# Performance work log

Measured on AMD Instinct MI355X. Metric: run time of the kernel, lower is better.

## Reference

```python
import jax, jax.numpy as jnp
import numpy as np

RATIO = 4


def setup_inputs() -> dict:
    key = jax.random.key(0)
    ks = jax.random.split(key, 6)
    b, c, hw = 8, 64, 256
    n = (hw // RATIO) ** 2  # 4096
    return {
        "x": jax.random.normal(ks[0], (b, c, hw, hw), dtype=jnp.float32),
        "weight": jax.random.normal(ks[1], (n, n), dtype=jnp.float32) * 0.01,
        "pih_w": jax.random.normal(ks[2], (c, c, 3, 3), dtype=jnp.float32) * 0.05,
        "pih_b": jax.random.normal(ks[3], (c,), dtype=jnp.float32) * 0.05,
        "up_w": jax.random.normal(ks[4], (c, c, 4, 4), dtype=jnp.float32) * 0.05,
        "up_b": jax.random.normal(ks[5], (c,), dtype=jnp.float32) * 0.05,
    }


def reference(x, weight, pih_w, pih_b, up_w, up_b):
    b, c, h, w = x.shape
    identity = x
    # MaxPool2d(ratio)
    xp = jax.lax.reduce_window(x, -jnp.inf, jax.lax.max,
                               (1, 1, RATIO, RATIO), (1, 1, RATIO, RATIO), 'VALID')
    # 3x3 conv, pad 1
    x_pih = jax.lax.conv_general_dilated(
        xp, pih_w, window_strides=(1, 1), padding='SAME',
        dimension_numbers=('NCHW', 'OIHW', 'NCHW')) + pih_b[None, :, None, None]
    x_pih = jax.nn.relu(x_pih).reshape(b, c, -1)  # [b, c, N]
    # F.normalize(p=2, dim=2)
    nrm = jnp.sqrt(jnp.sum(x_pih * x_pih, axis=2, keepdims=True))
    nx = x_pih / jnp.maximum(nrm, 1e-12)
    # channel-channel affinity [b, c, c]
    A = jnp.einsum('bcn,bdn->bcd', nx, nx)
    # vectorized D^{-1/2}, replacing per-batch torch.diag loop
    d = 1.0 / jnp.sqrt(jnp.sum(A, axis=2) + 1e-8)  # [b, c]
    d = jnp.where(jnp.isfinite(d), d, 0.0)
    L = jnp.eye(c, dtype=x.dtype)[None] - d[:, :, None] * A * d[:, None, :]
    # diffusion: L @ x_flat @ W
    xf = xp.reshape(b, c, -1)  # [b, c, N]
    out = jnp.einsum('bcd,bdn->bcn', L, xf)
    out = jnp.einsum('bcn,nm->bcm', out, weight)
    hp, wp = h // RATIO, w // RATIO
    out = out.reshape(b, c, hp, wp)
    # ConvTranspose2d(k=4, s=4): each pixel expands to a 4x4 block
    up = jnp.einsum('bchw,coij->bohiwj', out, up_w).reshape(b, c, h, w)
    up = up + up_b[None, :, None, None]
    return jax.nn.relu(up + identity)
```

## Files before the change

### kernel.cpp

```cpp
#include <hip/hip_runtime.h>

#define NB 8
#define NC 64
#define HW 256
#define HP 64
#define NN 4096

typedef unsigned short u16;
typedef unsigned int u32;
typedef __attribute__((ext_vector_type(8))) short s16x8;
typedef __attribute__((ext_vector_type(8))) unsigned short u16x8;
typedef __attribute__((ext_vector_type(4))) float f32x4;

__device__ __forceinline__ u16 f2bf(float f) {
    unsigned u = __float_as_uint(f);
    return (u16)((u + 0x7fffu + ((u >> 16) & 1u)) >> 16);
}
__device__ __forceinline__ float bf2f(u16 v) {
    return __uint_as_float(((unsigned)v) << 16);
}

#define GLOAD16(gsrc, ldst) \
    __builtin_amdgcn_global_load_lds((const __attribute__((address_space(1))) unsigned int*)(gsrc), \
                                     (__attribute__((address_space(3))) unsigned int*)(ldst), 16, 0, 0)

__global__ __launch_bounds__(256) void maxpool_nhwc_k(const float* __restrict__ x,
                                                      u16* __restrict__ xpc) {
    __shared__ u16 tile[64 * 66];
    int bid = blockIdx.x;
    int b = bid >> 6, y = bid & 63;
    int t = threadIdx.x;
    int cl  = t >> 3;
    int seg = t & 7;
#pragma unroll
    for (int pass = 0; pass < 2; ++pass) {
        int c = pass * 32 + cl;
        const float* p = x + ((long)(b * 64 + c) * 256 + y * 4) * 256 + seg * 32;
        float m[8];
#pragma unroll
        for (int i = 0; i < 8; ++i) m[i] = -3.4e38f;
#pragma unroll
        for (int r = 0; r < 4; ++r)
#pragma unroll
            for (int i = 0; i < 8; ++i) {
                float4 v = *(const float4*)(p + r * 256 + i * 4);
                m[i] = fmaxf(m[i], fmaxf(fmaxf(v.x, v.y), fmaxf(v.z, v.w)));
            }
#pragma unroll
        for (int i = 0; i < 8; ++i) tile[c * 66 + seg * 8 + i] = f2bf(m[i]);
    }
    __syncthreads();
    int xo = t >> 2, cp = t & 3;
    u16x8 o0, o1;
#pragma unroll
    for (int e = 0; e < 8; ++e) o0[e] = tile[(cp * 16 + e) * 66 + xo];
#pragma unroll
    for (int e = 0; e < 8; ++e) o1[e] = tile[(cp * 16 + 8 + e) * 66 + xo];
    u16* dst = xpc + ((long)(b * 4096 + y * 64 + xo)) * 64 + cp * 16;
    *(u16x8*)dst = o0;
    *(u16x8*)(dst + 8) = o1;
}

__global__ __launch_bounds__(256) void transWb_k(const float* __restrict__ W,
                                                 u16* __restrict__ WTb) {
    __shared__ float tile[64 * 65];
    int k0 = blockIdx.x * 64;
    int n0 = blockIdx.y * 64;
    int t = threadIdx.x;
#pragma unroll
    for (int i = 0; i < 4; ++i) {
        int idx = t + i * 256;
        int r  = idx >> 4;
        int c4 = (idx & 15) * 4;
        float4 v = *(const float4*)&W[(long)(k0 + r) * 4096 + n0 + c4];
        tile[(c4 + 0) * 65 + r] = v.x;
        tile[(c4 + 1) * 65 + r] = v.y;
        tile[(c4 + 2) * 65 + r] = v.z;
        tile[(c4 + 3) * 65 + r] = v.w;
    }
    __syncthreads();
#pragma unroll
    for (int i = 0; i < 2; ++i) {
        int chunk = t + i * 256;
        int nr = chunk >> 3;
        int kc = (chunk & 7) * 8;
        u16x8 o;
#pragma unroll
        for (int j = 0; j < 8; ++j) o[j] = f2bf(tile[nr * 65 + kc + j]);
        *(u16x8*)&WTb[(long)(n0 + nr) * 4096 + k0 + kc] = o;
    }
}

__global__ __launch_bounds__(256) void prep_k(const float* __restrict__ uw,
                                              const float* __restrict__ pw,
                                              u16* __restrict__ Wb,
                                              u16* __restrict__ Bpack) {
    int bid = blockIdx.x;
    int t = threadIdx.x;
    if (bid < 256) {
        int idx = bid * 256 + t;
        int c = idx & 63;
        int n = idx >> 6;
        int o = n >> 4, i = (n >> 2) & 3, j = n & 3;
        Wb[idx] = f2bf(uw[((c * 64 + o) * 4 + i) * 4 + j]);
    } else {
        int idx = (bid - 256) * 256 + t;
        if (idx >= 36864) return;
        int e = idx & 7, l = (idx >> 3) & 63, nf = (idx >> 9) & 3, s = idx >> 11;
        int ch = s & 1, kd = s >> 1;
        int dy = kd / 3, dx = kd % 3;
        int o  = nf * 16 + (l & 15);
        int ci = ch * 32 + (l >> 4) * 8 + e;
        Bpack[idx] = f2bf(pw[((o * 64 + ci) * 3 + dy) * 3 + dx]);
    }
}

__global__ __launch_bounds__(256) void convgram_k(const u16* __restrict__ xpc,
                                                  const u16* __restrict__ Bpack,
                                                  const float* __restrict__ pb,
                                                  float* __restrict__ G) {
    __shared__ alignas(16) u16 ldsIn[3 * 66 * 64];
    __shared__ alignas(16) u16 ldsX[64 * 64];
    int bid = blockIdx.x;
    int b = bid >> 6, y = bid & 63;
    int t = threadIdx.x;
    int w = t >> 6, l = t & 63;
    int lr = l & 15, ksub = l >> 4;

    if (t < 48) {
        int r = t >> 4, q = t & 15;
        int off = r * 8448 + (q < 8 ? q * 16 : 8320 + (q - 8) * 16);
        *(u16x8*)((char*)ldsIn + off) = (u16x8){0, 0, 0, 0, 0, 0, 0, 0};
    }
#pragma unroll
    for (int i = 0; i < 6; ++i) {
        int r  = i >> 1;
        int ya = y - 1 + r;
        int wro = (i & 1) * 4096 + t * 16;
        int dst = r * 8448 + 128 + wro;
        if (ya >= 0 && ya < 64) {
            int xsl = 1 + (wro >> 7);
            int srcoff = (wro & ~127) | ((wro & 127) ^ ((xsl & 7) << 4));
            GLOAD16((const char*)xpc + (long)(b * 64 + ya) * 8192 + srcoff,
                    (char*)ldsIn + dst);
        } else {
            *(u16x8*)((char*)ldsIn + dst) = (u16x8){0, 0, 0, 0, 0, 0, 0, 0};
        }
    }
    __syncthreads();

    f32x4 acc[4];
#pragma unroll
    for (int mf = 0; mf < 4; ++mf) acc[mf] = (f32x4){0.f, 0.f, 0.f, 0.f};

#pragma unroll
    for (int kd = 0; kd < 9; ++kd) {
        int dy = kd / 3, dx = kd % 3;
#pragma unroll
        for (int ch = 0; ch < 2; ++ch) {
            int s = kd * 2 + ch;
            s16x8 bfrag = *(const s16x8*)(Bpack + ((s * 4 + w) * 64 + l) * 8);
#pragma unroll
            for (int mf = 0; mf < 4; ++mf) {
                int xsl  = mf * 16 + lr + dx;
                int coff = (ch * 64 + ksub * 16) ^ ((xsl & 7) << 4);
                s16x8 af = *(const s16x8*)((const char*)ldsIn +
                                           dy * 8448 + xsl * 128 + coff);
                acc[mf] = __builtin_amdgcn_mfma_f32_16x16x32_bf16(
                    af, bfrag, acc[mf], 0, 0, 0);
            }
        }
    }
    int o = w * 16 + lr;
    float bias = pb[o];
#pragma unroll
    for (int mf = 0; mf < 4; ++mf)
#pragma unroll
        for (int rp = 0; rp < 2; ++rp) {
            u16 lo = f2bf(fmaxf(acc[mf][rp * 2]     + bias, 0.f));
            u16 hi = f2bf(fmaxf(acc[mf][rp * 2 + 1] + bias, 0.f));
            int nb   = (mf * 16 + ksub * 4 + rp * 2) * 2;
            int boff = nb ^ ((o & 7) << 4);
            *(u32*)((char*)ldsX + o * 128 + boff) = (u32)lo | ((u32)hi << 16);
        }
    __syncthreads();

    f32x4 g[4];
#pragma unroll
    for (int nf = 0; nf < 4; ++nf) g[nf] = (f32x4){0.f, 0.f, 0.f, 0.f};
#pragma unroll
    for (int kk = 0; kk < 2; ++kk) {
        int kb = kk * 64 + ksub * 16;
        int arow = w * 16 + lr;
        s16x8 af = *(const s16x8*)((const char*)ldsX + arow * 128 +
                                   (kb ^ ((arow & 7) << 4)));
#pragma unroll
        for (int nf = 0; nf < 4; ++nf) {
            int brow = nf * 16 + lr;
            s16x8 bf = *(const s16x8*)((const char*)ldsX + brow * 128 +
                                       (kb ^ ((brow & 7) << 4)));
            g[nf] = __builtin_amdgcn_mfma_f32_16x16x32_bf16(af, bf, g[nf], 0, 0, 0);
        }
    }
    float* Gb = G + b * 4096;
#pragma unroll
    for (int nf = 0; nf < 4; ++nf)
#pragma unroll
        for (int r = 0; r < 4; ++r)
            atomicAdd(&Gb[(w * 16 + ksub * 4 + r) * 64 + nf * 16 + lr], g[nf][r]);
}

__global__ __launch_bounds__(256) void diffuse_mfma_k(const float* __restrict__ G,
                                                      const u16* __restrict__ xpc,
                                                      u16* __restrict__ Ab16) {
    __shared__ alignas(16) u16 lds[128 * 64];
    __shared__ alignas(16) u16 ldsL[64 * 64];
    __shared__ float nrm[64], dvv[64];
    int n0 = blockIdx.x * 128;
    int b  = blockIdx.y;
    int t = threadIdx.x;
    int w = t >> 6, l = t & 63;
    int lr = l & 15, ksub = l >> 4;

#pragma unroll
    for (int i = 0; i < 4; ++i) {
        int d = i * 4096 + t * 16;
        int row = d >> 7, off = d & 127;
        GLOAD16((const char*)xpc + ((long)(b * 4096 + n0 + row)) * 128 +
                (off ^ ((row & 7) << 4)),
                (char*)lds + d);
    }

    const float* Gb = G + b * 4096;
    if (t < 64) nrm[t] = fmaxf(sqrtf(Gb[t * 64 + t]), 1e-12f);
    __syncthreads();
    if (t < 64) {
        float nc = nrm[t];
        float rs = 0.f;
        for (int d = 0; d < 64; ++d) rs += Gb[t * 64 + d] / (nc * nrm[d]);
        float dd = 1.0f / sqrtf(rs + 1e-8f);
        if (!(dd <= 3.0e38f)) dd = 0.0f;
        dvv[t] = dd;
    }
    __syncthreads();
    {
        int c = t >> 2;
        int dbase = (t & 3) * 16;
        float nc = nrm[c], dc = dvv[c];
#pragma unroll
        for (int dp2 = 0; dp2 < 8; ++dp2) {
            int d0 = dbase + dp2 * 2;
            float A0 = Gb[c * 64 + d0]     / (nc * nrm[d0]);
            float A1 = Gb[c * 64 + d0 + 1] / (nc * nrm[d0 + 1]);
            float v0 = ((c == d0)     ? 1.f : 0.f) - dc * A0 * dvv[d0];
            float v1 = ((c == d0 + 1) ? 1.f : 0.f) - dc * A1 * dvv[d0 + 1];
            int o = c * 64 + (d0 ^ ((c & 7) << 3));
            *(u32*)&ldsL[o] = (u32)f2bf(v0) | ((u32)f2bf(v1) << 16);
        }
    }
    __syncthreads();

    f32x4 acc[4][2];
#pragma unroll
    for (int mf = 0; mf < 4; ++mf)
#pragma unroll
        for (int nq = 0; nq < 2; ++nq) acc[mf][nq] = (f32x4){0.f, 0.f, 0.f, 0.f};

#pragma unroll
    for (int kk = 0; kk < 2; ++kk) {
        s16x8 bfr[2];
#pragma unroll
        for (int nq = 0; nq < 2; ++nq) {
            int brow = w * 32 + nq * 16 + lr;
            bfr[nq] = *(const s16x8*)((const char*)lds + brow * 128 +
                                      ((kk * 64 + ksub * 16) ^ ((brow & 7) << 4)));
        }
#pragma unroll
        for (int mf = 0; mf < 4; ++mf) {
            int arow = mf * 16 + lr;
            s16x8 af = *(const s16x8*)((const char*)ldsL + arow * 128 +
                                       ((kk * 64 + ksub * 16) ^ ((arow & 7) << 4)));
#pragma unroll
            for (int nq = 0; nq < 2; ++nq)
                acc[mf][nq] = __builtin_amdgcn_mfma_f32_16x16x32_bf16(
                    af, bfr[nq], acc[mf][nq], 0, 0, 0);
        }
    }
#pragma unroll
    for (int mf = 0; mf < 4; ++mf)
#pragma unroll
        for (int nq = 0; nq < 2; ++nq)
#pragma unroll
            for (int r = 0; r < 4; ++r)
                Ab16[((long)(b * 64 + mf * 16 + (l >> 4) * 4 + r)) * 4096 +
                     n0 + w * 32 + nq * 16 + lr] = f2bf(acc[mf][nq][r]);
}

#define KSPLIT 4
#define KSLICE 1024
__global__ __launch_bounds__(256) void gemm_mfma_k(const u16* __restrict__ A,
                                                   const u16* __restrict__ WT,
                                                   u16* __restrict__ Cp) {
    __shared__ alignas(16) u16 ldsA[8192];
    __shared__ alignas(16) u16 ldsB[8192];
    int bid = blockIdx.x;
    int swz = (bid & 7) * 64 + (bid >> 3);
    int m0 = (swz & 3) * 128;
    int n0 = ((swz >> 2) & 31) * 128;
    int z  = swz >> 7;
    int t = threadIdx.x;
    int w = t >> 6, l = t & 63;
    int wr = w >> 1, wc = w & 1;
    int lr = l & 15;
    int lk = (l >> 4) << 4;

    f32x4 acc[4][4];
#pragma unroll
    for (int mf = 0; mf < 4; ++mf)
#pragma unroll
        for (int nf = 0; nf < 4; ++nf) acc[mf][nf] = (f32x4){0.f, 0.f, 0.f, 0.f};

    const char* Ab = (const char*)(A  + (long)m0 * 4096 + z * KSLICE);
    const char* Bb = (const char*)(WT + (long)n0 * 4096 + z * KSLICE);

    for (int k0 = 0; k0 < KSLICE; k0 += 64) {
        __syncthreads();
#pragma unroll
        for (int i = 0; i < 4; ++i) {
            int d   = i * 4096 + t * 16;
            int row = d >> 7;
            int off = d & 127;
            int sk  = off ^ ((row & 7) << 4);
            GLOAD16(Ab + (long)row * 8192 + k0 * 2 + sk, (char*)ldsA + d);
            GLOAD16(Bb + (long)row * 8192 + k0 * 2 + sk, (char*)ldsB + d);
        }
        __syncthreads();
#pragma unroll
        for (int kk = 0; kk < 2; ++kk) {
            s16x8 af[4], bf[4];
#pragma unroll
            for (int f = 0; f < 4; ++f) {
                int ar = wr * 64 + f * 16 + lr;
                af[f] = *(const s16x8*)((const char*)ldsA + ar * 128 +
                                        ((kk * 64 + lk) ^ ((ar & 7) << 4)));
                int br = wc * 64 + f * 16 + lr;
                bf[f] = *(const s16x8*)((const char*)ldsB + br * 128 +
                                        ((kk * 64 + lk) ^ ((br & 7) << 4)));
            }
#pragma unroll
            for (int mf = 0; mf < 4; ++mf)
#pragma unroll
                for (int nf = 0; nf < 4; ++nf)
                    acc[mf][nf] = __builtin_amdgcn_mfma_f32_16x16x32_bf16(
                        af[mf], bf[nf], acc[mf][nf], 0, 0, 0);
        }
    }
    int tile = (swz & 3) * 32 + ((swz >> 2) & 31);
    u16 carr[64];
#pragma unroll
    for (int mf = 0; mf < 4; ++mf)
#pragma unroll
        for (int nf = 0; nf < 4; ++nf)
#pragma unroll
            for (int r = 0; r < 4; ++r)
                carr[mf * 16 + nf * 4 + r] = f2bf(acc[mf][nf][r]);
    u16* dp = Cp + ((long)(z * 128 + tile) * 256 + t) * 64;
#pragma unroll
    for (int v8 = 0; v8 < 8; ++v8)
        *(u16x8*)&dp[v8 * 8] = *(const u16x8*)&carr[v8 * 8];
}

__global__ __launch_bounds__(256) void reduce4T_k(const u16* __restrict__ Cp,
                                                  u16* __restrict__ A2) {
    __shared__ u16 ldsT[128 * 128];
    int tile = blockIdx.x;
    int tm = tile >> 5, tn = tile & 31;
    int n0 = tn * 128;
    int t = threadIdx.x;
    int w = t >> 6, l = t & 63;
    int wr = w >> 1, wc = w & 1, lr = l & 15;

    float s[64];
#pragma unroll
    for (int k = 0; k < 64; ++k) s[k] = 0.f;

    const u16* dp = Cp + ((long)tile * 256 + t) * 64;
#pragma unroll
    for (int z = 0; z < KSPLIT; ++z) {
        const u16* pz = dp + (long)z * 128 * 256 * 64;
#pragma unroll
        for (int v8 = 0; v8 < 8; ++v8) {
            u16x8 vv = *(const u16x8*)&pz[v8 * 8];
#pragma unroll
            for (int e = 0; e < 8; ++e) s[v8 * 8 + e] += bf2f(vv[e]);
        }
    }
#pragma unroll
    for (int mf = 0; mf < 4; ++mf)
#pragma unroll
        for (int nf = 0; nf < 4; ++nf) {
            int mbase = wr * 64 + mf * 16 + (l >> 4) * 4;
            int pix   = wc * 64 + nf * 16 + lr;
            int g = (mbase >> 3) ^ (pix & 7);
            int o = pix * 128 + g * 8 + (mbase & 7);
            u32 w0 = (u32)f2bf(s[mf * 16 + nf * 4 + 0]) |
                     ((u32)f2bf(s[mf * 16 + nf * 4 + 1]) << 16);
            u32 w1 = (u32)f2bf(s[mf * 16 + nf * 4 + 2]) |
                     ((u32)f2bf(s[mf * 16 + nf * 4 + 3]) << 16);
            *(u32*)&ldsT[o]     = w0;
            *(u32*)&ldsT[o + 2] = w1;
        }
    __syncthreads();
    int pix_l = t >> 1, bh = t & 1;
    u16* dst = A2 + ((long)((2 * tm + bh) * 4096 + n0 + pix_l)) * 64;
#pragma unroll
    for (int gg = 0; gg < 8; ++gg) {
        int q = bh * 8 + gg;
        u16x8 vv = *(const u16x8*)&ldsT[pix_l * 128 + (q ^ (pix_l & 7)) * 8];
        *(u16x8*)&dst[gg * 8] = vv;
    }
}

__global__ __launch_bounds__(256) void convT_mfma_k(const u16* __restrict__ A2,
                                                    const u16* __restrict__ Wb,
                                                    const float* __restrict__ ub,
                                                    const float* __restrict__ x,
                                                    float* __restrict__ out) {
    __shared__ alignas(16) char smem[34816];
    u16*   ldsA = (u16*)smem;
    u16*   ldsB = (u16*)(smem + 16384);
    float* ldsC = (float*)smem;
    int mt = blockIdx.x;
    int nt = blockIdx.y;
    int m0 = mt * 128;
    int n0 = nt * 128;
    int t = threadIdx.x;
    int w = t >> 6, l = t & 63;
    int wr = w >> 1, wc = w & 1;
    int lr = l & 15;
    int lkb = (l >> 4) << 4;

    const char* Ab = (const char*)(A2 + (long)m0 * 64);
    const char* Bb = (const char*)(Wb + (long)n0 * 64);
#pragma unroll
    for (int i = 0; i < 4; ++i) {
        int d = i * 4096 + t * 16;
        int srcoff = (d & ~127) | ((d & 127) ^ (((d >> 7) & 7) << 4));
        GLOAD16(Ab + srcoff, (char*)ldsA + d);
        GLOAD16(Bb + srcoff, (char*)ldsB + d);
    }
    __syncthreads();

    f32x4 acc[4][4];
#pragma unroll
    for (int mf = 0; mf < 4; ++mf)
#pragma unroll
        for (int nf = 0; nf < 4; ++nf) acc[mf][nf] = (f32x4){0.f, 0.f, 0.f, 0.f};

#pragma unroll
    for (int kk = 0; kk < 2; ++kk) {
        s16x8 af[4], bfg[4];
#pragma unroll
        for (int f = 0; f < 4; ++f) {
            int ar = wr * 64 + f * 16 + lr;
            af[f] = *(const s16x8*)((const char*)ldsA + ar * 128 +
                                    ((kk * 64 + lkb) ^ ((ar & 7) << 4)));
            int br = wc * 64 + f * 16 + lr;
            bfg[f] = *(const s16x8*)((const char*)ldsB + br * 128 +
                                     ((kk * 64 + lkb) ^ ((br & 7) << 4)));
        }
#pragma unroll
        for (int mf = 0; mf < 4; ++mf)
#pragma unroll
            for (int nf = 0; nf < 4; ++nf)
                acc[mf][nf] = __builtin_amdgcn_mfma_f32_16x16x32_bf16(
                    af[mf], bfg[nf], acc[mf][nf], 0, 0, 0);
    }
    __syncthreads();

#pragma unroll
    for (int nh = 0; nh < 2; ++nh) {
        if (nh) __syncthreads();
        if (wc == nh) {
#pragma unroll
            for (int mf = 0; mf < 4; ++mf)
#pragma unroll
                for (int nf = 0; nf < 4; ++nf)
#pragma unroll
                    for (int r = 0; r < 4; ++r) {
                        int row = wr * 64 + mf * 16 + (l >> 4) * 4 + r;
                        int col = nf * 16 + lr;
                        ldsC[row * 68 + (col ^ (((row >> 3) & 7) << 2))] =
                            acc[mf][nf][r];
                    }
        }
        __syncthreads();
#pragma unroll
        for (int q = 0; q < 2; ++q) {
            int idx = q * 256 + t;
            int ml = idx & 127;
            int oo = idx >> 7;
            int o  = nt * 8 + nh * 4 + oo;
            float bias = ub[o];
            int mg = m0 + ml;
            int b = mg >> 12, pix = mg & 4095;
            int h = pix >> 6, ww = pix & 63;
            long base = ((long)(b * 64 + o) * 256 + h * 4) * 256 + ww * 4;
#pragma unroll
            for (int i = 0; i < 4; ++i) {
                f32x4 cv = *(const f32x4*)&ldsC[ml * 68 +
                            ((oo * 16 + i * 4) ^ (((ml >> 3) & 7) << 2))];
                float4 xi = *(const float4*)&x[base + i * 256];
                float4 rr;
                rr.x = fmaxf(cv[0] + bias + xi.x, 0.f);
                rr.y = fmaxf(cv[1] + bias + xi.y, 0.f);
                rr.z = fmaxf(cv[2] + bias + xi.z, 0.f);
                rr.w = fmaxf(cv[3] + bias + xi.w, 0.f);
                *(float4*)&out[base + i * 256] = rr;
            }
        }
    }
}

extern "C" void kernel_launch(void* const* d_in, const int* in_sizes, int n_in,
                              void* d_out, int out_size, void* d_ws, size_t ws_size,
                              hipStream_t stream) {
    const float* x      = (const float*)d_in[0];
    const float* weight = (const float*)d_in[1];
    const float* pih_w  = (const float*)d_in[2];
    const float* pih_b  = (const float*)d_in[3];
    const float* up_w   = (const float*)d_in[4];
    const float* up_b   = (const float*)d_in[5];
    float* out = (float*)d_out;
    float* ws  = (float*)d_ws;

    u16*   xpc   = (u16*)ws;
    u16*   Ab16  = (u16*)(ws + 3145728);
    float* G     = ws + 4194304;
    u16*   Wb    = (u16*)(ws + 4259840);
    u16*   WTb   = (u16*)(ws + 4325376);
    u16*   Cp    = (u16*)(ws + 12713984);
    u16*   Bpack = Cp + 2097152;
    u16*   A2    = (u16*)ws;

    hipMemsetAsync(G, 0, 32768 * sizeof(float), stream);
    maxpool_nhwc_k<<<512, 256, 0, stream>>>(x, xpc);
    transWb_k     <<<dim3(64, 64), 256, 0, stream>>>(weight, WTb);
    prep_k        <<<400, 256, 0, stream>>>(up_w, pih_w, Wb, Bpack);
    convgram_k    <<<512, 256, 0, stream>>>(xpc, Bpack, pih_b, G);
    diffuse_mfma_k<<<dim3(32, 8), 256, 0, stream>>>(G, xpc, Ab16);
    gemm_mfma_k   <<<512, 256, 0, stream>>>(Ab16, WTb, Cp);
    reduce4T_k    <<<128, 256, 0, stream>>>(Cp, A2);
    convT_mfma_k  <<<dim3(256, 8), 256, 0, stream>>>(A2, Wb, up_b, x, out);
}
```

Before: 168.0 us.

## Merge prep kernels into one launch and fold split-K reduction into convT

Merges the maxpool, weight transpose and parameter-packing kernels into a single launch that picks its role from the block index. Removes the separate split-K reduce/transpose kernel: each convT block now sums the bf16 partial products straight from the Cp buffer and writes the swizzled A tile into LDS, so the A2 intermediate is no longer written and read back. Adds a block-index swizzle to the convT grid, which would otherwise read each Cp tile repeatedly across the 8 n-tiles; the swizzle is meant to keep those re-reads close together in time so they hit cache. The trade-off is that the split-K partials are now re-read by every n-tile block instead of once.

```diff
diff --git a/kernel.cpp b/kernel.cpp
--- a/kernel.cpp
+++ b/kernel.cpp
@@ -24,94 +24,94 @@
     __builtin_amdgcn_global_load_lds((const __attribute__((address_space(1))) unsigned int*)(gsrc), \
                                      (__attribute__((address_space(3))) unsigned int*)(ldst), 16, 0, 0)
 
-__global__ __launch_bounds__(256) void maxpool_nhwc_k(const float* __restrict__ x,
-                                                      u16* __restrict__ xpc) {
-    __shared__ u16 tile[64 * 66];
-    int bid = blockIdx.x;
-    int b = bid >> 6, y = bid & 63;
-    int t = threadIdx.x;
-    int cl  = t >> 3;
-    int seg = t & 7;
-#pragma unroll
-    for (int pass = 0; pass < 2; ++pass) {
-        int c = pass * 32 + cl;
-        const float* p = x + ((long)(b * 64 + c) * 256 + y * 4) * 256 + seg * 32;
-        float m[8];
-#pragma unroll
-        for (int i = 0; i < 8; ++i) m[i] = -3.4e38f;
-#pragma unroll
-        for (int r = 0; r < 4; ++r)
-#pragma unroll
-            for (int i = 0; i < 8; ++i) {
-                float4 v = *(const float4*)(p + r * 256 + i * 4);
-                m[i] = fmaxf(m[i], fmaxf(fmaxf(v.x, v.y), fmaxf(v.z, v.w)));
-            }
-#pragma unroll
-        for (int i = 0; i < 8; ++i) tile[c * 66 + seg * 8 + i] = f2bf(m[i]);
-    }
-    __syncthreads();
-    int xo = t >> 2, cp = t & 3;
-    u16x8 o0, o1;
-#pragma unroll
-    for (int e = 0; e < 8; ++e) o0[e] = tile[(cp * 16 + e) * 66 + xo];
-#pragma unroll
-    for (int e = 0; e < 8; ++e) o1[e] = tile[(cp * 16 + 8 + e) * 66 + xo];
-    u16* dst = xpc + ((long)(b * 4096 + y * 64 + xo)) * 64 + cp * 16;
-    *(u16x8*)dst = o0;
-    *(u16x8*)(dst + 8) = o1;
-}
-
-__global__ __launch_bounds__(256) void transWb_k(const float* __restrict__ W,
-                                                 u16* __restrict__ WTb) {
-    __shared__ float tile[64 * 65];
-    int k0 = blockIdx.x * 64;
-    int n0 = blockIdx.y * 64;
-    int t = threadIdx.x;
-#pragma unroll
-    for (int i = 0; i < 4; ++i) {
-        int idx = t + i * 256;
-        int r  = idx >> 4;
-        int c4 = (idx & 15) * 4;
-        float4 v = *(const float4*)&W[(long)(k0 + r) * 4096 + n0 + c4];
-        tile[(c4 + 0) * 65 + r] = v.x;
-        tile[(c4 + 1) * 65 + r] = v.y;
-        tile[(c4 + 2) * 65 + r] = v.z;
-        tile[(c4 + 3) * 65 + r] = v.w;
-    }
-    __syncthreads();
-#pragma unroll
-    for (int i = 0; i < 2; ++i) {
-        int chunk = t + i * 256;
-        int nr = chunk >> 3;
-        int kc = (chunk & 7) * 8;
-        u16x8 o;
-#pragma unroll
-        for (int j = 0; j < 8; ++j) o[j] = f2bf(tile[nr * 65 + kc + j]);
-        *(u16x8*)&WTb[(long)(n0 + nr) * 4096 + k0 + kc] = o;
-    }
-}
-
-__global__ __launch_bounds__(256) void prep_k(const float* __restrict__ uw,
-                                              const float* __restrict__ pw,
-                                              u16* __restrict__ Wb,
-                                              u16* __restrict__ Bpack) {
+__global__ __launch_bounds__(256) void front_k(const float* __restrict__ x,
+                                               const float* __restrict__ W,
+                                               const float* __restrict__ uw,
+                                               const float* __restrict__ pw,
+                                               u16* __restrict__ xpc,
+                                               u16* __restrict__ WTb,
+                                               u16* __restrict__ Wb,
+                                               u16* __restrict__ Bpack) {
+    __shared__ alignas(16) char sm[16640];
     int bid = blockIdx.x;
     int t = threadIdx.x;
-    if (bid < 256) {
-        int idx = bid * 256 + t;
-        int c = idx & 63;
-        int n = idx >> 6;
-        int o = n >> 4, i = (n >> 2) & 3, j = n & 3;
-        Wb[idx] = f2bf(uw[((c * 64 + o) * 4 + i) * 4 + j]);
+    if (bid < 512) {
+        u16* tile = (u16*)sm;
+        int b = bid >> 6, y = bid & 63;
+        int cl  = t >> 3;
+        int seg = t & 7;
+#pragma unroll
+        for (int pass = 0; pass < 2; ++pass) {
+            int c = pass * 32 + cl;
+            const float* p = x + ((long)(b * 64 + c) * 256 + y * 4) * 256 + seg * 32;
+            float m[8];
+#pragma unroll
+            for (int i = 0; i < 8; ++i) m[i] = -3.4e38f;
+#pragma unroll
+            for (int r = 0; r < 4; ++r)
+#pragma unroll
+                for (int i = 0; i < 8; ++i) {
+                    float4 v = *(const float4*)(p + r * 256 + i * 4);
+                    m[i] = fmaxf(m[i], fmaxf(fmaxf(v.x, v.y), fmaxf(v.z, v.w)));
+                }
+#pragma unroll
+            for (int i = 0; i < 8; ++i) tile[c * 66 + seg * 8 + i] = f2bf(m[i]);
+        }
+        __syncthreads();
+        int xo = t >> 2, cp = t & 3;
+        u16x8 o0, o1;
+#pragma unroll
+        for (int e = 0; e < 8; ++e) o0[e] = tile[(cp * 16 + e) * 66 + xo];
+#pragma unroll
+        for (int e = 0; e < 8; ++e) o1[e] = tile[(cp * 16 + 8 + e) * 66 + xo];
+        u16* dst = xpc + ((long)(b * 4096 + y * 64 + xo)) * 64 + cp * 16;
+        *(u16x8*)dst = o0;
+        *(u16x8*)(dst + 8) = o1;
+    } else if (bid < 4608) {
+        float* tile = (float*)sm;
+        int tb = bid - 512;
+        int k0 = (tb & 63) * 64;
+        int n0 = (tb >> 6) * 64;
+#pragma unroll
+        for (int i = 0; i < 4; ++i) {
+            int idx = t + i * 256;
+            int r  = idx >> 4;
+            int c4 = (idx & 15) * 4;
+            float4 v = *(const float4*)&W[(long)(k0 + r) * 4096 + n0 + c4];
+            tile[(c4 + 0) * 65 + r] = v.x;
+            tile[(c4 + 1) * 65 + r] = v.y;
+            tile[(c4 + 2) * 65 + r] = v.z;
+            tile[(c4 + 3) * 65 + r] = v.w;
+        }
+        __syncthreads();
+#pragma unroll
+        for (int i = 0; i < 2; ++i) {
+            int chunk = t + i * 256;
+            int nr = chunk >> 3;
+            int kc = (chunk & 7) * 8;
+            u16x8 o;
+#pragma unroll
+            for (int j = 0; j < 8; ++j) o[j] = f2bf(tile[nr * 65 + kc + j]);
+            *(u16x8*)&WTb[(long)(n0 + nr) * 4096 + k0 + kc] = o;
+        }
     } else {
-        int idx = (bid - 256) * 256 + t;
-        if (idx >= 36864) return;
-        int e = idx & 7, l = (idx >> 3) & 63, nf = (idx >> 9) & 3, s = idx >> 11;
-        int ch = s & 1, kd = s >> 1;
-        int dy = kd / 3, dx = kd % 3;
-        int o  = nf * 16 + (l & 15);
-        int ci = ch * 32 + (l >> 4) * 8 + e;
-        Bpack[idx] = f2bf(pw[((o * 64 + ci) * 3 + dy) * 3 + dx]);
+        int pbid = bid - 4608;
+        if (pbid < 256) {
+            int idx = pbid * 256 + t;
+            int c = idx & 63;
+            int n = idx >> 6;
+            int o = n >> 4, i = (n >> 2) & 3, j = n & 3;
+            Wb[idx] = f2bf(uw[((c * 64 + o) * 4 + i) * 4 + j]);
+        } else {
+            int idx = (pbid - 256) * 256 + t;
+            if (idx >= 36864) return;
+            int e = idx & 7, l = (idx >> 3) & 63, nf = (idx >> 9) & 3, s = idx >> 11;
+            int ch = s & 1, kd = s >> 1;
+            int dy = kd / 3, dx = kd % 3;
+            int o  = nf * 16 + (l & 15);
+            int ci = ch * 32 + (l >> 4) * 8 + e;
+            Bpack[idx] = f2bf(pw[((o * 64 + ci) * 3 + dy) * 3 + dx]);
+        }
     }
 }
 
@@ -370,58 +370,7 @@
         *(u16x8*)&dp[v8 * 8] = *(const u16x8*)&carr[v8 * 8];
 }
 
-__global__ __launch_bounds__(256) void reduce4T_k(const u16* __restrict__ Cp,
-                                                  u16* __restrict__ A2) {
-    __shared__ u16 ldsT[128 * 128];
-    int tile = blockIdx.x;
-    int tm = tile >> 5, tn = tile & 31;
-    int n0 = tn * 128;
-    int t = threadIdx.x;
-    int w = t >> 6, l = t & 63;
-    int wr = w >> 1, wc = w & 1, lr = l & 15;
-
-    float s[64];
-#pragma unroll
-    for (int k = 0; k < 64; ++k) s[k] = 0.f;
-
-    const u16* dp = Cp + ((long)tile * 256 + t) * 64;
-#pragma unroll
-    for (int z = 0; z < KSPLIT; ++z) {
-        const u16* pz = dp + (long)z * 128 * 256 * 64;
-#pragma unroll
-        for (int v8 = 0; v8 < 8; ++v8) {
-            u16x8 vv = *(const u16x8*)&pz[v8 * 8];
-#pragma unroll
-            for (int e = 0; e < 8; ++e) s[v8 * 8 + e] += bf2f(vv[e]);
-        }
-    }
-#pragma unroll
-    for (int mf = 0; mf < 4; ++mf)
-#pragma unroll
-        for (int nf = 0; nf < 4; ++nf) {
-            int mbase = wr * 64 + mf * 16 + (l >> 4) * 4;
-            int pix   = wc * 64 + nf * 16 + lr;
-            int g = (mbase >> 3) ^ (pix & 7);
-            int o = pix * 128 + g * 8 + (mbase & 7);
-            u32 w0 = (u32)f2bf(s[mf * 16 + nf * 4 + 0]) |
-                     ((u32)f2bf(s[mf * 16 + nf * 4 + 1]) << 16);
-            u32 w1 = (u32)f2bf(s[mf * 16 + nf * 4 + 2]) |
-                     ((u32)f2bf(s[mf * 16 + nf * 4 + 3]) << 16);
-            *(u32*)&ldsT[o]     = w0;
-            *(u32*)&ldsT[o + 2] = w1;
-        }
-    __syncthreads();
-    int pix_l = t >> 1, bh = t & 1;
-    u16* dst = A2 + ((long)((2 * tm + bh) * 4096 + n0 + pix_l)) * 64;
-#pragma unroll
-    for (int gg = 0; gg < 8; ++gg) {
-        int q = bh * 8 + gg;
-        u16x8 vv = *(const u16x8*)&ldsT[pix_l * 128 + (q ^ (pix_l & 7)) * 8];
-        *(u16x8*)&dst[gg * 8] = vv;
-    }
-}
-
-__global__ __launch_bounds__(256) void convT_mfma_k(const u16* __restrict__ A2,
+__global__ __launch_bounds__(256) void convT_mfma_k(const u16* __restrict__ Cp,
                                                     const u16* __restrict__ Wb,
                                                     const float* __restrict__ ub,
                                                     const float* __restrict__ x,
@@ -430,8 +379,10 @@
     u16*   ldsA = (u16*)smem;
     u16*   ldsB = (u16*)(smem + 16384);
     float* ldsC = (float*)smem;
-    int mt = blockIdx.x;
-    int nt = blockIdx.y;
+    int bid = blockIdx.x;
+    int swzb = (bid & 7) * 256 + (bid >> 3);
+    int mt = swzb >> 3;
+    int nt = swzb & 7;
     int m0 = mt * 128;
     int n0 = nt * 128;
     int t = threadIdx.x;
@@ -440,14 +391,53 @@
     int lr = l & 15;
     int lkb = (l >> 4) << 4;
 
-    const char* Ab = (const char*)(A2 + (long)m0 * 64);
     const char* Bb = (const char*)(Wb + (long)n0 * 64);
 #pragma unroll
     for (int i = 0; i < 4; ++i) {
         int d = i * 4096 + t * 16;
         int srcoff = (d & ~127) | ((d & 127) ^ (((d >> 7) & 7) << 4));
-        GLOAD16(Ab + srcoff, (char*)ldsA + d);
         GLOAD16(Bb + srcoff, (char*)ldsB + d);
+    }
+
+    {
+        int b_   = mt >> 5;
+        int wr_g = b_ & 1;
+        int tile_g = (b_ >> 1) * 32 + (mt & 31);
+        int tg = wr_g * 128 + (t & 127);
+        int h  = t >> 7;
+        int l_g = tg & 63, wc_g = (tg >> 6) & 1;
+        int k4 = l_g >> 4, lr_g = l_g & 15;
+        float s[32];
+#pragma unroll
+        for (int k = 0; k < 32; ++k) s[k] = 0.f;
+        const u16* dpb = Cp + ((long)tile_g * 256 + tg) * 64 + h * 32;
+#pragma unroll
+        for (int z = 0; z < KSPLIT; ++z) {
+            const u16* pz = dpb + (long)z * 2097152;
+#pragma unroll
+            for (int j = 0; j < 4; ++j) {
+                u16x8 vv = *(const u16x8*)&pz[j * 8];
+#pragma unroll
+                for (int e = 0; e < 8; ++e) s[j * 8 + e] += bf2f(vv[e]);
+            }
+        }
+#pragma unroll
+        for (int j = 0; j < 4; ++j) {
+            int v8 = h * 4 + j;
+            int mf = v8 >> 1;
+            int c0 = mf * 16 + k4 * 4;
+#pragma unroll
+            for (int q = 0; q < 2; ++q) {
+                int nf  = (v8 & 1) * 2 + q;
+                int pix = wc_g * 64 + nf * 16 + lr_g;
+                int sw  = (pix & 7) << 4;
+                int f   = j * 8 + q * 4;
+                u32 w0 = (u32)f2bf(s[f + 0]) | ((u32)f2bf(s[f + 1]) << 16);
+                u32 w1 = (u32)f2bf(s[f + 2]) | ((u32)f2bf(s[f + 3]) << 16);
+                *(u32*)((char*)ldsA + pix * 128 + ((c0 * 2) ^ sw))     = w0;
+                *(u32*)((char*)ldsA + pix * 128 + ((c0 * 2 + 4) ^ sw)) = w1;
+            }
+        }
     }
     __syncthreads();
 
@@ -504,8 +494,8 @@
             float bias = ub[o];
             int mg = m0 + ml;
             int b = mg >> 12, pix = mg & 4095;
-            int h = pix >> 6, ww = pix & 63;
-            long base = ((long)(b * 64 + o) * 256 + h * 4) * 256 + ww * 4;
+            int h2 = pix >> 6, ww = pix & 63;
+            long base = ((long)(b * 64 + o) * 256 + h2 * 4) * 256 + ww * 4;
 #pragma unroll
             for (int i = 0; i < 4; ++i) {
                 f32x4 cv = *(const f32x4*)&ldsC[ml * 68 +
@@ -541,15 +531,12 @@
     u16*   WTb   = (u16*)(ws + 4325376);
     u16*   Cp    = (u16*)(ws + 12713984);
     u16*   Bpack = Cp + 2097152;
-    u16*   A2    = (u16*)ws;
 
     hipMemsetAsync(G, 0, 32768 * sizeof(float), stream);
-    maxpool_nhwc_k<<<512, 256, 0, stream>>>(x, xpc);
-    transWb_k     <<<dim3(64, 64), 256, 0, stream>>>(weight, WTb);
-    prep_k        <<<400, 256, 0, stream>>>(up_w, pih_w, Wb, Bpack);
+    front_k       <<<5008, 256, 0, stream>>>(x, weight, up_w, pih_w,
+                                             xpc, WTb, Wb, Bpack);
     convgram_k    <<<512, 256, 0, stream>>>(xpc, Bpack, pih_b, G);
     diffuse_mfma_k<<<dim3(32, 8), 256, 0, stream>>>(G, xpc, Ab16);
     gemm_mfma_k   <<<512, 256, 0, stream>>>(Ab16, WTb, Cp);
-    reduce4T_k    <<<128, 256, 0, stream>>>(Cp, A2);
-    convT_mfma_k  <<<dim3(256, 8), 256, 0, stream>>>(A2, Wb, up_b, x, out);
-}
+    convT_mfma_k  <<<2048, 256, 0, stream>>>(Cp, Wb, up_b, x, out);
+}
```

New measurement: 160.7 us. 1.05x faster.

## Merge maxpool, weight transpose and prep into one front kernel; swizzle convT grid

Applied to the files above, without the earlier changes.

Folds the three independent preprocessing kernels (maxpool to NHWC bf16, weight transpose to bf16, and conv/convT weight packing) into one launch that dispatches by block index range. The weight transpose now uses 128x128 tiles with an XOR-swizzled bf16 LDS tile, packing to bf16 before staging, in place of the fp32 padded tile. The convT kernel moves to a 1D grid whose block-to-tile mapping is remapped so that blocks running at the same time spread over more M tiles. The aim is to cut launch gaps and the transpose's LDS traffic, at the cost of a heterogeneous kernel whose shared-memory footprint is sized for its largest branch.

```diff
diff --git a/kernel.cpp b/kernel.cpp
--- a/kernel.cpp
+++ b/kernel.cpp
@@ -10,6 +10,7 @@
 typedef unsigned int u32;
 typedef __attribute__((ext_vector_type(8))) short s16x8;
 typedef __attribute__((ext_vector_type(8))) unsigned short u16x8;
+typedef __attribute__((ext_vector_type(4))) unsigned short u16x4;
 typedef __attribute__((ext_vector_type(4))) float f32x4;
 
 __device__ __forceinline__ u16 f2bf(float f) {
@@ -24,94 +25,100 @@
     __builtin_amdgcn_global_load_lds((const __attribute__((address_space(1))) unsigned int*)(gsrc), \
                                      (__attribute__((address_space(3))) unsigned int*)(ldst), 16, 0, 0)
 
-__global__ __launch_bounds__(256) void maxpool_nhwc_k(const float* __restrict__ x,
-                                                      u16* __restrict__ xpc) {
-    __shared__ u16 tile[64 * 66];
-    int bid = blockIdx.x;
-    int b = bid >> 6, y = bid & 63;
-    int t = threadIdx.x;
-    int cl  = t >> 3;
-    int seg = t & 7;
-#pragma unroll
-    for (int pass = 0; pass < 2; ++pass) {
-        int c = pass * 32 + cl;
-        const float* p = x + ((long)(b * 64 + c) * 256 + y * 4) * 256 + seg * 32;
-        float m[8];
-#pragma unroll
-        for (int i = 0; i < 8; ++i) m[i] = -3.4e38f;
-#pragma unroll
-        for (int r = 0; r < 4; ++r)
-#pragma unroll
-            for (int i = 0; i < 8; ++i) {
-                float4 v = *(const float4*)(p + r * 256 + i * 4);
-                m[i] = fmaxf(m[i], fmaxf(fmaxf(v.x, v.y), fmaxf(v.z, v.w)));
-            }
-#pragma unroll
-        for (int i = 0; i < 8; ++i) tile[c * 66 + seg * 8 + i] = f2bf(m[i]);
-    }
-    __syncthreads();
-    int xo = t >> 2, cp = t & 3;
-    u16x8 o0, o1;
-#pragma unroll
-    for (int e = 0; e < 8; ++e) o0[e] = tile[(cp * 16 + e) * 66 + xo];
-#pragma unroll
-    for (int e = 0; e < 8; ++e) o1[e] = tile[(cp * 16 + 8 + e) * 66 + xo];
-    u16* dst = xpc + ((long)(b * 4096 + y * 64 + xo)) * 64 + cp * 16;
-    *(u16x8*)dst = o0;
-    *(u16x8*)(dst + 8) = o1;
-}
-
-__global__ __launch_bounds__(256) void transWb_k(const float* __restrict__ W,
-                                                 u16* __restrict__ WTb) {
-    __shared__ float tile[64 * 65];
-    int k0 = blockIdx.x * 64;
-    int n0 = blockIdx.y * 64;
-    int t = threadIdx.x;
-#pragma unroll
-    for (int i = 0; i < 4; ++i) {
-        int idx = t + i * 256;
-        int r  = idx >> 4;
-        int c4 = (idx & 15) * 4;
-        float4 v = *(const float4*)&W[(long)(k0 + r) * 4096 + n0 + c4];
-        tile[(c4 + 0) * 65 + r] = v.x;
-        tile[(c4 + 1) * 65 + r] = v.y;
-        tile[(c4 + 2) * 65 + r] = v.z;
-        tile[(c4 + 3) * 65 + r] = v.w;
-    }
-    __syncthreads();
-#pragma unroll
-    for (int i = 0; i < 2; ++i) {
-        int chunk = t + i * 256;
-        int nr = chunk >> 3;
-        int kc = (chunk & 7) * 8;
-        u16x8 o;
-#pragma unroll
-        for (int j = 0; j < 8; ++j) o[j] = f2bf(tile[nr * 65 + kc + j]);
-        *(u16x8*)&WTb[(long)(n0 + nr) * 4096 + k0 + kc] = o;
-    }
-}
-
-__global__ __launch_bounds__(256) void prep_k(const float* __restrict__ uw,
-                                              const float* __restrict__ pw,
-                                              u16* __restrict__ Wb,
-                                              u16* __restrict__ Bpack) {
+__global__ __launch_bounds__(256) void front_k(const float* __restrict__ x,
+                                               const float* __restrict__ W,
+                                               const float* __restrict__ uw,
+                                               const float* __restrict__ pw,
+                                               u16* __restrict__ xpc,
+                                               u16* __restrict__ WTb,
+                                               u16* __restrict__ Wb,
+                                               u16* __restrict__ Bpack) {
+    __shared__ alignas(16) char sm[32768];
     int bid = blockIdx.x;
     int t = threadIdx.x;
-    if (bid < 256) {
-        int idx = bid * 256 + t;
-        int c = idx & 63;
-        int n = idx >> 6;
-        int o = n >> 4, i = (n >> 2) & 3, j = n & 3;
-        Wb[idx] = f2bf(uw[((c * 64 + o) * 4 + i) * 4 + j]);
+    if (bid < 512) {
+        u16* tile = (u16*)sm;
+        int b = bid >> 6, y = bid & 63;
+        int cl  = t >> 3;
+        int seg = t & 7;
+#pragma unroll
+        for (int pass = 0; pass < 2; ++pass) {
+            int c = pass * 32 + cl;
+            const float* p = x + ((long)(b * 64 + c) * 256 + y * 4) * 256 + seg * 32;
+            float m[8];
+#pragma unroll
+            for (int i = 0; i < 8; ++i) m[i] = -3.4e38f;
+#pragma unroll
+            for (int r = 0; r < 4; ++r)
+#pragma unroll
+                for (int i = 0; i < 8; ++i) {
+                    float4 v = *(const float4*)(p + r * 256 + i * 4);
+                    m[i] = fmaxf(m[i], fmaxf(fmaxf(v.x, v.y), fmaxf(v.z, v.w)));
+                }
+#pragma unroll
+            for (int i = 0; i < 8; ++i) tile[c * 66 + seg * 8 + i] = f2bf(m[i]);
+        }
+        __syncthreads();
+        int xo = t >> 2, cp = t & 3;
+        u16x8 o0, o1;
+#pragma unroll
+        for (int e = 0; e < 8; ++e) o0[e] = tile[(cp * 16 + e) * 66 + xo];
+#pragma unroll
+        for (int e = 0; e < 8; ++e) o1[e] = tile[(cp * 16 + 8 + e) * 66 + xo];
+        u16* dst = xpc + ((long)(b * 4096 + y * 64 + xo)) * 64 + cp * 16;
+        *(u16x8*)dst = o0;
+        *(u16x8*)(dst + 8) = o1;
+    } else if (bid < 1536) {
+        u16* tile = (u16*)sm;
+        int tb = bid - 512;
+        int k0 = (tb >> 5) * 128;
+        int n0 = (tb & 31) * 128;
+        int nq = t & 31;
+#pragma unroll
+        for (int p = 0; p < 4; ++p) {
+            int kq = (t >> 5) + p * 8;
+            float4 v[4];
+#pragma unroll
+            for (int j = 0; j < 4; ++j)
+                v[j] = *(const float4*)&W[(long)(k0 + kq * 4 + j) * 4096 + n0 + nq * 4];
+#pragma unroll
+            for (int jn = 0; jn < 4; ++jn) {
+                int n = nq * 4 + jn;
+                u16x4 c4;
+                c4[0] = f2bf(((const float*)&v[0])[jn]);
+                c4[1] = f2bf(((const float*)&v[1])[jn]);
+                c4[2] = f2bf(((const float*)&v[2])[jn]);
+                c4[3] = f2bf(((const float*)&v[3])[jn]);
+                *(u16x4*)((char*)tile + n * 256 + ((kq * 8) ^ ((n & 15) << 4))) = c4;
+            }
+        }
+        __syncthreads();
+#pragma unroll
+        for (int q = 0; q < 8; ++q) {
+            int chunk = t + q * 256;
+            int n = chunk >> 4, seg = chunk & 15;
+            u16x8 o = *(const u16x8*)((const char*)tile + n * 256 +
+                                      ((seg * 16) ^ ((n & 15) << 4)));
+            *(u16x8*)&WTb[(long)(n0 + n) * 4096 + k0 + seg * 8] = o;
+        }
     } else {
-        int idx = (bid - 256) * 256 + t;
-        if (idx >= 36864) return;
-        int e = idx & 7, l = (idx >> 3) & 63, nf = (idx >> 9) & 3, s = idx >> 11;
-        int ch = s & 1, kd = s >> 1;
-        int dy = kd / 3, dx = kd % 3;
-        int o  = nf * 16 + (l & 15);
-        int ci = ch * 32 + (l >> 4) * 8 + e;
-        Bpack[idx] = f2bf(pw[((o * 64 + ci) * 3 + dy) * 3 + dx]);
+        int pbid = bid - 1536;
+        if (pbid < 256) {
+            int idx = pbid * 256 + t;
+            int c = idx & 63;
+            int n = idx >> 6;
+            int o = n >> 4, i = (n >> 2) & 3, j = n & 3;
+            Wb[idx] = f2bf(uw[((c * 64 + o) * 4 + i) * 4 + j]);
+        } else {
+            int idx = (pbid - 256) * 256 + t;
+            if (idx >= 36864) return;
+            int e = idx & 7, l = (idx >> 3) & 63, nf = (idx >> 9) & 3, s = idx >> 11;
+            int ch = s & 1, kd = s >> 1;
+            int dy = kd / 3, dx = kd % 3;
+            int o  = nf * 16 + (l & 15);
+            int ci = ch * 32 + (l >> 4) * 8 + e;
+            Bpack[idx] = f2bf(pw[((o * 64 + ci) * 3 + dy) * 3 + dx]);
+        }
     }
 }
 
@@ -387,7 +394,7 @@
     const u16* dp = Cp + ((long)tile * 256 + t) * 64;
 #pragma unroll
     for (int z = 0; z < KSPLIT; ++z) {
-        const u16* pz = dp + (long)z * 128 * 256 * 64;
+        const u16* pz = dp + (long)z * 2097152;
 #pragma unroll
         for (int v8 = 0; v8 < 8; ++v8) {
             u16x8 vv = *(const u16x8*)&pz[v8 * 8];
@@ -430,8 +437,10 @@
     u16*   ldsA = (u16*)smem;
     u16*   ldsB = (u16*)(smem + 16384);
     float* ldsC = (float*)smem;
-    int mt = blockIdx.x;
-    int nt = blockIdx.y;
+    int bid = blockIdx.x;
+    int swzb = (bid & 7) * 256 + (bid >> 3);
+    int mt = swzb >> 3;
+    int nt = swzb & 7;
     int m0 = mt * 128;
     int n0 = nt * 128;
     int t = threadIdx.x;
@@ -504,8 +513,8 @@
             float bias = ub[o];
             int mg = m0 + ml;
             int b = mg >> 12, pix = mg & 4095;
-            int h = pix >> 6, ww = pix & 63;
-            long base = ((long)(b * 64 + o) * 256 + h * 4) * 256 + ww * 4;
+            int h2 = pix >> 6, ww = pix & 63;
+            long base = ((long)(b * 64 + o) * 256 + h2 * 4) * 256 + ww * 4;
 #pragma unroll
             for (int i = 0; i < 4; ++i) {
                 f32x4 cv = *(const f32x4*)&ldsC[ml * 68 +
@@ -544,12 +553,11 @@
     u16*   A2    = (u16*)ws;
 
     hipMemsetAsync(G, 0, 32768 * sizeof(float), stream);
-    maxpool_nhwc_k<<<512, 256, 0, stream>>>(x, xpc);
-    transWb_k     <<<dim3(64, 64), 256, 0, stream>>>(weight, WTb);
-    prep_k        <<<400, 256, 0, stream>>>(up_w, pih_w, Wb, Bpack);
+    front_k       <<<1936, 256, 0, stream>>>(x, weight, up_w, pih_w,
+                                             xpc, WTb, Wb, Bpack);
     convgram_k    <<<512, 256, 0, stream>>>(xpc, Bpack, pih_b, G);
     diffuse_mfma_k<<<dim3(32, 8), 256, 0, stream>>>(G, xpc, Ab16);
     gemm_mfma_k   <<<512, 256, 0, stream>>>(Ab16, WTb, Cp);
     reduce4T_k    <<<128, 256, 0, stream>>>(Cp, A2);
-    convT_mfma_k  <<<dim3(256, 8), 256, 0, stream>>>(A2, Wb, up_b, x, out);
-}
+    convT_mfma_k  <<<2048, 256, 0, stream>>>(A2, Wb, up_b, x, out);
+}
```

Result: faster. 156.7 us (-6.7%).
